# Kernel tuning notes

Measured on AMD Instinct MI355X. Metric: run time of the kernel, lower is better.

Reference implementation:

```python
import jax, jax.numpy as jnp
import numpy as np

N_NODES = 50000


def gcn_conv(x, src, dst, W, b, n_nodes):
    # x: [N, Fin]; src/dst: [E'] (self-loops already included)
    # PyG GCNConv: h = x @ W; aggregate with norm = deg^{-1/2}[src] * deg^{-1/2}[dst]; + bias
    ones = jnp.ones(src.shape[0], dtype=x.dtype)
    deg = jax.ops.segment_sum(ones, dst, num_segments=n_nodes)  # [N]
    dinv = jnp.where(deg > 0, jax.lax.rsqrt(deg), 0.0)
    norm = dinv[src] * dinv[dst]  # [E']
    h = x @ W  # [N, Fout]
    msgs = h[src] * norm[:, None]  # gather + scale, [E', Fout]
    out = jax.ops.segment_sum(msgs, dst, num_segments=n_nodes)  # scatter-add
    return out + b


def setup_inputs() -> dict:
    key = jax.random.key(0)
    ks = jax.random.split(key, 8)
    n, e = N_NODES, 800000
    in_c, out_c = 64, 32
    hid = 2 * out_c  # 64

    def glorot(k, fan_in, fan_out):
        s = jnp.sqrt(2.0 / (fan_in + fan_out))
        return jax.random.normal(k, (fan_in, fan_out), dtype=jnp.float32) * s

    return {
        "z": jax.random.normal(ks[0], (n, in_c), dtype=jnp.float32),
        "edge_index": jax.random.randint(ks[1], (2, e), 0, n, dtype=jnp.int32),
        "W1": glorot(ks[2], in_c, hid),
        "b1": jnp.zeros((hid,), dtype=jnp.float32),
        "W2": glorot(ks[3], hid, out_c),
        "b2": jnp.zeros((out_c,), dtype=jnp.float32),
        "Wfc": glorot(ks[4], out_c, 1024),
        "bfc": jnp.zeros((1024,), dtype=jnp.float32),
    }


def reference(z, edge_index, W1, b1, W2, b2, Wfc, bfc):
    n = z.shape[0]
    # add self-loops once (same augmented graph used by both convs)
    loops = jnp.arange(n, dtype=edge_index.dtype)
    src = jnp.concatenate([edge_index[0], loops])
    dst = jnp.concatenate([edge_index[1], loops])

    h = jax.nn.relu(gcn_conv(z, src, dst, W1, b1, n))
    h = gcn_conv(h, src, dst, W2, b2, n)
    return h @ Wfc + bfc
```

## Files before the change

kernel.cpp:

```cpp
#include <hip/hip_runtime.h>


#define TB 256
#define FC_ROWS 32
#define SCHUNK 4096
#define FLAGB (1 << 30)

typedef __attribute__((ext_vector_type(2))) float f32x2;

__device__ __forceinline__ unsigned short f2bf(float f) {
    unsigned u = __float_as_uint(f);
    u += 0x7fffu + ((u >> 16) & 1u);
    return (unsigned short)(u >> 16);
}

__device__ __forceinline__ void bf4_accum(uint2 p, float4& a) {
    a.x += __uint_as_float(p.x << 16);
    a.y += __uint_as_float(p.x & 0xffff0000u);
    a.z += __uint_as_float(p.y << 16);
    a.w += __uint_as_float(p.y & 0xffff0000u);
}


__global__ void k_zero(int4* __restrict__ p, int n4) {
    int i = blockIdx.x * TB + threadIdx.x;
    if (i < n4) p[i] = make_int4(0, 0, 0, 0);
}


__global__ void k_hist(const int* __restrict__ dst, int* __restrict__ cnt,
                       int* __restrict__ slot, int E) {
    int e = blockIdx.x * TB + threadIdx.x;
    if (e < E) slot[e] = atomicAdd(&cnt[dst[e]], 1);
}

__global__ __launch_bounds__(1024)
void k_scanLB(const int* __restrict__ cnt, int* __restrict__ off,
              float* __restrict__ dinv, int* __restrict__ work, int n, int E) {
    __shared__ int wsum[16];
    __shared__ int pfx_s;
    int b = blockIdx.x;
    int i4 = b * SCHUNK + threadIdx.x * 4;
    int lane = threadIdx.x & 63, wid = threadIdx.x >> 6;
    int v0 = 0, v1 = 0, v2 = 0, v3 = 0;
    if (i4 + 3 < n) {
        int4 t = *(const int4*)(cnt + i4);
        v0 = t.x; v1 = t.y; v2 = t.z; v3 = t.w;
    } else {
        if (i4 < n) v0 = cnt[i4];
        if (i4 + 1 < n) v1 = cnt[i4 + 1];
        if (i4 + 2 < n) v2 = cnt[i4 + 2];
        if (i4 + 3 < n) v3 = cnt[i4 + 3];
    }
    if (i4 < n)     dinv[i4]     = rsqrtf((float)(v0 + 1));
    if (i4 + 1 < n) dinv[i4 + 1] = rsqrtf((float)(v1 + 1));
    if (i4 + 2 < n) dinv[i4 + 2] = rsqrtf((float)(v2 + 1));
    if (i4 + 3 < n) dinv[i4 + 3] = rsqrtf((float)(v3 + 1));

    int s = v0 + v1 + v2 + v3;
    int x = s;
#pragma unroll
    for (int ofs = 1; ofs < 64; ofs <<= 1) {
        int t = __shfl_up(x, ofs, 64);
        if (lane >= ofs) x += t;
    }
    if (lane == 63) wsum[wid] = x;
    __syncthreads();
    int wp = 0;
#pragma unroll
    for (int wv = 0; wv < 16; ++wv) wp += (wv < wid) ? wsum[wv] : 0;
    int excl = wp + x - s;

    if (threadIdx.x == 0) {
        int tot = 0;
#pragma unroll
        for (int wv = 0; wv < 16; ++wv) tot += wsum[wv];
        atomicOr(&work[b], tot | FLAGB);
        int pfx = 0;
        for (int j = 0; j < b; ++j) {
            int v;
            do { v = atomicOr(&work[j], 0); } while (!(v & FLAGB));
            pfx += v & (FLAGB - 1);
        }
        pfx_s = pfx;
        if (b == 0) off[n] = E;
    }
    __syncthreads();
    excl += pfx_s;
    if (i4 < n)     off[i4]     = excl;
    if (i4 + 1 < n) off[i4 + 1] = excl + v0;
    if (i4 + 2 < n) off[i4 + 2] = excl + v0 + v1;
    if (i4 + 3 < n) off[i4 + 3] = excl + v0 + v1 + v2;
}

__global__ void k_fill_gemm(const int* __restrict__ src, const int* __restrict__ dst,
                            const int* __restrict__ off, const int* __restrict__ slot,
                            int* __restrict__ eSrc, int E, int fillBlocks,
                            const float* __restrict__ X, const float* __restrict__ W,
                            const float* __restrict__ dinv,
                            unsigned short* __restrict__ Y, int n) {
    __shared__ float Ws[64 * 64];
    __shared__ float Xs[16 * 64];
    if ((int)blockIdx.x < fillBlocks) {
        int e = blockIdx.x * TB + threadIdx.x;
        if (e < E) eSrc[off[dst[e]] + slot[e]] = src[e];
        return;
    }
    int gb = blockIdx.x - fillBlocks;
    for (int i = threadIdx.x; i < 64 * 64; i += TB) Ws[i] = W[i];
    int r0 = gb * 16;
    int rows = min(16, n - r0);
    {
        const float4* Xg = (const float4*)(X + (size_t)r0 * 64);
        float4* Xs4 = (float4*)Xs;
        int tot4 = rows * 16;
        for (int i = threadIdx.x; i < tot4; i += TB) Xs4[i] = Xg[i];
    }
    __syncthreads();
    int c = threadIdx.x & 63;
    int g = threadIdx.x >> 6;
#pragma unroll
    for (int rr = 0; rr < 4; ++rr) {
        int rb = g + rr * 4;
        int r = r0 + rb;
        if (r >= n) break;
        const float* x = Xs + rb * 64;
        float acc = 0.f;
#pragma unroll
        for (int k = 0; k < 64; ++k) acc = fmaf(x[k], Ws[k * 64 + c], acc);
        Y[(size_t)r * 64 + c] = f2bf(acc * dinv[r]);
    }
}


__global__ void k_gemm_64_32(const float* __restrict__ X, const float* __restrict__ W,
                             const float* __restrict__ dinv,
                             unsigned short* __restrict__ Y, int n) {
    __shared__ float Ws[64 * 32];
    __shared__ float Xs[32 * 64];
    for (int i = threadIdx.x; i < 64 * 32; i += TB) Ws[i] = W[i];
    int r0 = blockIdx.x * 32;
    int rows = min(32, n - r0);
    {
        const float4* Xg = (const float4*)(X + (size_t)r0 * 64);
        float4* Xs4 = (float4*)Xs;
        int tot4 = rows * 16;
        for (int i = threadIdx.x; i < tot4; i += TB) Xs4[i] = Xg[i];
    }
    __syncthreads();
    int c = threadIdx.x & 31;
    int g = threadIdx.x >> 5;
#pragma unroll
    for (int rr = 0; rr < 4; ++rr) {
        int rb = g + rr * 8;
        int r = r0 + rb;
        if (r >= n) break;
        const float* x = Xs + rb * 64;
        float acc = 0.f;
#pragma unroll
        for (int k = 0; k < 64; ++k) acc = fmaf(x[k], Ws[k * 32 + c], acc);
        Y[(size_t)r * 32 + c] = f2bf(acc * dinv[r]);
    }
}


__global__ void k_agg64(const uint2* __restrict__ H2, const int* __restrict__ off,
                        const int* __restrict__ eSrc, const float* __restrict__ dinv,
                        const float4* __restrict__ b4, float4* __restrict__ out4, int n) {
    int node = blockIdx.x * 16 + (threadIdx.x >> 4);
    if (node >= n) return;
    int feat4 = threadIdx.x & 15;
    int j0 = off[node], j1 = off[node + 1];
    float4 a0 = make_float4(0.f, 0.f, 0.f, 0.f);
    float4 a1 = make_float4(0.f, 0.f, 0.f, 0.f);
    float4 a2 = make_float4(0.f, 0.f, 0.f, 0.f);
    float4 a3 = make_float4(0.f, 0.f, 0.f, 0.f);
    int e = j0;
    for (; e + 4 <= j1; e += 4) {
        int s0 = eSrc[e], s1 = eSrc[e + 1], s2 = eSrc[e + 2], s3 = eSrc[e + 3];
        uint2 v0 = H2[(size_t)s0 * 16 + feat4];
        uint2 v1 = H2[(size_t)s1 * 16 + feat4];
        uint2 v2 = H2[(size_t)s2 * 16 + feat4];
        uint2 v3 = H2[(size_t)s3 * 16 + feat4];
        bf4_accum(v0, a0);
        bf4_accum(v1, a1);
        bf4_accum(v2, a2);
        bf4_accum(v3, a3);
    }
    for (; e < j1; ++e) bf4_accum(H2[(size_t)eSrc[e] * 16 + feat4], a0);
    float4 self = make_float4(0.f, 0.f, 0.f, 0.f);
    bf4_accum(H2[(size_t)node * 16 + feat4], self);
    float dv = dinv[node];
    float4 bb = b4[feat4];
    float4 r;
    r.x = fmaxf(fmaf((a0.x + a1.x) + (a2.x + a3.x) + self.x, dv, bb.x), 0.f);
    r.y = fmaxf(fmaf((a0.y + a1.y) + (a2.y + a3.y) + self.y, dv, bb.y), 0.f);
    r.z = fmaxf(fmaf((a0.z + a1.z) + (a2.z + a3.z) + self.z, dv, bb.z), 0.f);
    r.w = fmaxf(fmaf((a0.w + a1.w) + (a2.w + a3.w) + self.w, dv, bb.w), 0.f);
    out4[(size_t)node * 16 + feat4] = r;
}

__global__ void k_agg32(const uint2* __restrict__ H2, const int* __restrict__ off,
                        const int* __restrict__ eSrc, const float* __restrict__ dinv,
                        const float4* __restrict__ b4, float4* __restrict__ out4, int n) {
    int node = blockIdx.x * 32 + (threadIdx.x >> 3);
    if (node >= n) return;
    int feat4 = threadIdx.x & 7;
    int j0 = off[node], j1 = off[node + 1];
    float4 a0 = make_float4(0.f, 0.f, 0.f, 0.f);
    float4 a1 = make_float4(0.f, 0.f, 0.f, 0.f);
    float4 a2 = make_float4(0.f, 0.f, 0.f, 0.f);
    float4 a3 = make_float4(0.f, 0.f, 0.f, 0.f);
    int e = j0;
    for (; e + 4 <= j1; e += 4) {
        int s0 = eSrc[e], s1 = eSrc[e + 1], s2 = eSrc[e + 2], s3 = eSrc[e + 3];
        uint2 v0 = H2[(size_t)s0 * 8 + feat4];
        uint2 v1 = H2[(size_t)s1 * 8 + feat4];
        uint2 v2 = H2[(size_t)s2 * 8 + feat4];
        uint2 v3 = H2[(size_t)s3 * 8 + feat4];
        bf4_accum(v0, a0);
        bf4_accum(v1, a1);
        bf4_accum(v2, a2);
        bf4_accum(v3, a3);
    }
    for (; e < j1; ++e) bf4_accum(H2[(size_t)eSrc[e] * 8 + feat4], a0);
    float4 self = make_float4(0.f, 0.f, 0.f, 0.f);
    bf4_accum(H2[(size_t)node * 8 + feat4], self);
    float dv = dinv[node];
    float4 bb = b4[feat4];
    float4 r;
    r.x = fmaf((a0.x + a1.x) + (a2.x + a3.x) + self.x, dv, bb.x);
    r.y = fmaf((a0.y + a1.y) + (a2.y + a3.y) + self.y, dv, bb.y);
    r.z = fmaf((a0.z + a1.z) + (a2.z + a3.z) + self.z, dv, bb.z);
    r.w = fmaf((a0.w + a1.w) + (a2.w + a3.w) + self.w, dv, bb.w);
    out4[(size_t)node * 8 + feat4] = r;
}

__global__ __launch_bounds__(TB, 4)
void k_fc2(const float* __restrict__ X, const float* __restrict__ W,
           const float* __restrict__ bias, float* __restrict__ Y, int n) {
    __shared__ float Xs[FC_ROWS * 32];
    int c0 = blockIdx.x * 512 + threadIdx.x * 2;
    int r0 = blockIdx.y * FC_ROWS;
    int rows = min(FC_ROWS, n - r0);

    f32x2 w[32];
#pragma unroll
    for (int k = 0; k < 32; ++k) w[k] = *(const f32x2*)(W + k * 1024 + c0);
    f32x2 bb = *(const f32x2*)(bias + c0);

    {
        const float4* Xg = (const float4*)(X + (size_t)r0 * 32);
        float4* Xs4 = (float4*)Xs;
        int tot4 = rows * 8;
        for (int i = threadIdx.x; i < tot4; i += TB) Xs4[i] = Xg[i];
    }
    __syncthreads();

    for (int r = 0; r < rows; ++r) {
        const float* x = Xs + r * 32;
        float a0 = bb.x, a1 = bb.y;
#pragma unroll
        for (int k = 0; k < 32; ++k) {
            float xv = x[k];
            a0 = fmaf(xv, w[k].x, a0);
            a1 = fmaf(xv, w[k].y, a1);
        }
        f32x2 v;
        v.x = a0; v.y = a1;
        __builtin_nontemporal_store(v, (f32x2*)(Y + (size_t)(r0 + r) * 1024 + c0));
    }
}


extern "C" void kernel_launch(void* const* d_in, const int* in_sizes, int n_in,
                              void* d_out, int out_size, void* d_ws, size_t ws_size,
                              hipStream_t stream) {
    const float* z   = (const float*)d_in[0];
    const int*   ei  = (const int*)d_in[1];
    const float* W1  = (const float*)d_in[2];
    const float* b1  = (const float*)d_in[3];
    const float* W2  = (const float*)d_in[4];
    const float* b2  = (const float*)d_in[5];
    const float* Wfc = (const float*)d_in[6];
    const float* bfc = (const float*)d_in[7];
    float* out = (float*)d_out;

    int n = in_sizes[0] / 64;
    int E = in_sizes[1] / 2;
    const int* src = ei;
    const int* dst = ei + E;

    int nPad = (n + 3) & ~3;
    int* cnt    = (int*)d_ws;
    int* work   = cnt + nPad;
    int* off    = work + 16;
    int* slot   = off + ((n + 1 + 3) & ~3);
    int* eSrc   = slot + E;
    float* dinv = (float*)(eSrc + E);
    unsigned short* h1b = (unsigned short*)(dinv + n);
    float* bufB = (float*)(dinv + n + (size_t)n * 32);
    unsigned short* h2b = (unsigned short*)(bufB + (size_t)n * 64);
    float* agg2 = bufB + (size_t)n * 64 + (size_t)n * 16;

    int nChunks = (n + SCHUNK - 1) / SCHUNK;

    {
        int n4 = (nPad + 16) / 4;
        k_zero<<<(n4 + TB - 1) / TB, TB, 0, stream>>>((int4*)cnt, n4);
    }
    k_hist<<<(E + TB - 1) / TB, TB, 0, stream>>>(dst, cnt, slot, E);
    k_scanLB<<<nChunks, 1024, 0, stream>>>(cnt, off, dinv, work, n, E);

    {
        int fillBlocks = (E + TB - 1) / TB;
        int gemmBlocks = (n + 15) / 16;
        k_fill_gemm<<<fillBlocks + gemmBlocks, TB, 0, stream>>>(
            src, dst, off, slot, eSrc, E, fillBlocks, z, W1, dinv, h1b, n);
    }

    k_agg64<<<(n + 15) / 16, TB, 0, stream>>>((const uint2*)h1b, off, eSrc, dinv,
                                              (const float4*)b1, (float4*)bufB, n);

    k_gemm_64_32<<<(n + 31) / 32, TB, 0, stream>>>(bufB, W2, dinv, h2b, n);
    k_agg32<<<(n + 31) / 32, TB, 0, stream>>>((const uint2*)h2b, off, eSrc, dinv,
                                              (const float4*)b2, (float4*)agg2, n);

    {
        dim3 grid(2, (n + FC_ROWS - 1) / FC_ROWS);
        k_fc2<<<grid, TB, 0, stream>>>(agg2, Wfc, bfc, out, n);
    }
}
```

Baseline: 186.7 us.

## Fuse layer-1 aggregation with W2 GEMM and layer-2 aggregation with FC

The first aggregation now computes its ReLU'd rows into shared memory and immediately applies the 64x32 W2 projection, writing bf16 h2 directly. The second aggregation writes its 32-wide rows into shared memory and the same 512-thread block then computes the 1024-column output projection. This removes two intermediate fp32 buffers and two kernel launches. In exchange, each block serializes its gather phase before its dense phase, and the FC block shape changes to 512 threads covering all columns for 64 rows.

```diff
diff --git a/kernel.cpp b/kernel.cpp
--- a/kernel.cpp
+++ b/kernel.cpp
@@ -2,7 +2,7 @@
 
 
 #define TB 256
-#define FC_ROWS 32
+#define FCTB 512
 #define SCHUNK 4096
 #define FLAGB (1 << 30)
 
@@ -132,131 +132,103 @@
     }
 }
 
-
-__global__ void k_gemm_64_32(const float* __restrict__ X, const float* __restrict__ W,
-                             const float* __restrict__ dinv,
-                             unsigned short* __restrict__ Y, int n) {
-    __shared__ float Ws[64 * 32];
-    __shared__ float Xs[32 * 64];
-    for (int i = threadIdx.x; i < 64 * 32; i += TB) Ws[i] = W[i];
-    int r0 = blockIdx.x * 32;
-    int rows = min(32, n - r0);
-    {
-        const float4* Xg = (const float4*)(X + (size_t)r0 * 64);
-        float4* Xs4 = (float4*)Xs;
-        int tot4 = rows * 16;
-        for (int i = threadIdx.x; i < tot4; i += TB) Xs4[i] = Xg[i];
-    }
-    __syncthreads();
-    int c = threadIdx.x & 31;
-    int g = threadIdx.x >> 5;
-#pragma unroll
-    for (int rr = 0; rr < 4; ++rr) {
-        int rb = g + rr * 8;
-        int r = r0 + rb;
-        if (r >= n) break;
-        const float* x = Xs + rb * 64;
-        float acc = 0.f;
-#pragma unroll
-        for (int k = 0; k < 64; ++k) acc = fmaf(x[k], Ws[k * 32 + c], acc);
-        Y[(size_t)r * 32 + c] = f2bf(acc * dinv[r]);
-    }
-}
-
-
-__global__ void k_agg64(const uint2* __restrict__ H2, const int* __restrict__ off,
-                        const int* __restrict__ eSrc, const float* __restrict__ dinv,
-                        const float4* __restrict__ b4, float4* __restrict__ out4, int n) {
-    int node = blockIdx.x * 16 + (threadIdx.x >> 4);
-    if (node >= n) return;
+__global__ void k_agg64g2(const uint2* __restrict__ H2, const int* __restrict__ off,
+                          const int* __restrict__ eSrc, const float* __restrict__ dinv,
+                          const float4* __restrict__ b4, const float* __restrict__ W2,
+                          unsigned short* __restrict__ h2b, int n) {
+    __shared__ float rowsS[16 * 64];
+    __shared__ float W2s[64 * 32];
+    for (int i = threadIdx.x; i < 64 * 32; i += TB) W2s[i] = W2[i];
+    int r0 = blockIdx.x * 16;
+    int node = r0 + (threadIdx.x >> 4);
     int feat4 = threadIdx.x & 15;
-    int j0 = off[node], j1 = off[node + 1];
-    float4 a0 = make_float4(0.f, 0.f, 0.f, 0.f);
-    float4 a1 = make_float4(0.f, 0.f, 0.f, 0.f);
-    float4 a2 = make_float4(0.f, 0.f, 0.f, 0.f);
-    float4 a3 = make_float4(0.f, 0.f, 0.f, 0.f);
-    int e = j0;
-    for (; e + 4 <= j1; e += 4) {
-        int s0 = eSrc[e], s1 = eSrc[e + 1], s2 = eSrc[e + 2], s3 = eSrc[e + 3];
-        uint2 v0 = H2[(size_t)s0 * 16 + feat4];
-        uint2 v1 = H2[(size_t)s1 * 16 + feat4];
-        uint2 v2 = H2[(size_t)s2 * 16 + feat4];
-        uint2 v3 = H2[(size_t)s3 * 16 + feat4];
-        bf4_accum(v0, a0);
-        bf4_accum(v1, a1);
-        bf4_accum(v2, a2);
-        bf4_accum(v3, a3);
-    }
-    for (; e < j1; ++e) bf4_accum(H2[(size_t)eSrc[e] * 16 + feat4], a0);
-    float4 self = make_float4(0.f, 0.f, 0.f, 0.f);
-    bf4_accum(H2[(size_t)node * 16 + feat4], self);
-    float dv = dinv[node];
-    float4 bb = b4[feat4];
-    float4 r;
-    r.x = fmaxf(fmaf((a0.x + a1.x) + (a2.x + a3.x) + self.x, dv, bb.x), 0.f);
-    r.y = fmaxf(fmaf((a0.y + a1.y) + (a2.y + a3.y) + self.y, dv, bb.y), 0.f);
-    r.z = fmaxf(fmaf((a0.z + a1.z) + (a2.z + a3.z) + self.z, dv, bb.z), 0.f);
-    r.w = fmaxf(fmaf((a0.w + a1.w) + (a2.w + a3.w) + self.w, dv, bb.w), 0.f);
-    out4[(size_t)node * 16 + feat4] = r;
-}
-
-__global__ void k_agg32(const uint2* __restrict__ H2, const int* __restrict__ off,
-                        const int* __restrict__ eSrc, const float* __restrict__ dinv,
-                        const float4* __restrict__ b4, float4* __restrict__ out4, int n) {
-    int node = blockIdx.x * 32 + (threadIdx.x >> 3);
-    if (node >= n) return;
+    if (node < n) {
+        int j0 = off[node], j1 = off[node + 1];
+        float4 a0 = make_float4(0.f, 0.f, 0.f, 0.f);
+        float4 a1 = make_float4(0.f, 0.f, 0.f, 0.f);
+        float4 a2 = make_float4(0.f, 0.f, 0.f, 0.f);
+        float4 a3 = make_float4(0.f, 0.f, 0.f, 0.f);
+        int e = j0;
+        for (; e + 4 <= j1; e += 4) {
+            int s0 = eSrc[e], s1 = eSrc[e + 1], s2 = eSrc[e + 2], s3 = eSrc[e + 3];
+            bf4_accum(H2[(size_t)s0 * 16 + feat4], a0);
+            bf4_accum(H2[(size_t)s1 * 16 + feat4], a1);
+            bf4_accum(H2[(size_t)s2 * 16 + feat4], a2);
+            bf4_accum(H2[(size_t)s3 * 16 + feat4], a3);
+        }
+        for (; e < j1; ++e) bf4_accum(H2[(size_t)eSrc[e] * 16 + feat4], a0);
+        float4 self = make_float4(0.f, 0.f, 0.f, 0.f);
+        bf4_accum(H2[(size_t)node * 16 + feat4], self);
+        float dv = dinv[node];
+        float4 bb = b4[feat4];
+        float4 r;
+        r.x = fmaxf(fmaf((a0.x + a1.x) + (a2.x + a3.x) + self.x, dv, bb.x), 0.f);
+        r.y = fmaxf(fmaf((a0.y + a1.y) + (a2.y + a3.y) + self.y, dv, bb.y), 0.f);
+        r.z = fmaxf(fmaf((a0.z + a1.z) + (a2.z + a3.z) + self.z, dv, bb.z), 0.f);
+        r.w = fmaxf(fmaf((a0.w + a1.w) + (a2.w + a3.w) + self.w, dv, bb.w), 0.f);
+        ((float4*)rowsS)[(threadIdx.x >> 4) * 16 + feat4] = r;
+    }
+    __syncthreads();
+#pragma unroll
+    for (int rep = 0; rep < 2; ++rep) {
+        int idx = rep * TB + threadIdx.x;
+        int nd = idx >> 5, c = idx & 31;
+        int gn = r0 + nd;
+        if (gn < n) {
+            const float* x = rowsS + nd * 64;
+            float acc = 0.f;
+#pragma unroll
+            for (int k = 0; k < 64; ++k) acc = fmaf(x[k], W2s[k * 32 + c], acc);
+            h2b[(size_t)gn * 32 + c] = f2bf(acc * dinv[gn]);
+        }
+    }
+}
+
+__global__ __launch_bounds__(FCTB, 4)
+void k_aggfc(const uint2* __restrict__ H2, const int* __restrict__ off,
+             const int* __restrict__ eSrc, const float* __restrict__ dinv,
+             const float4* __restrict__ b4, const float* __restrict__ Wfc,
+             const float* __restrict__ bfc, float* __restrict__ Y, int n) {
+    __shared__ float Xs[64 * 32];
+    int r0 = blockIdx.x * 64;
+    int c0 = threadIdx.x * 2;
+
+    f32x2 w[32];
+#pragma unroll
+    for (int k = 0; k < 32; ++k) w[k] = *(const f32x2*)(Wfc + k * 1024 + c0);
+    f32x2 bb = *(const f32x2*)(bfc + c0);
+
+    int node = r0 + (threadIdx.x >> 3);
     int feat4 = threadIdx.x & 7;
-    int j0 = off[node], j1 = off[node + 1];
-    float4 a0 = make_float4(0.f, 0.f, 0.f, 0.f);
-    float4 a1 = make_float4(0.f, 0.f, 0.f, 0.f);
-    float4 a2 = make_float4(0.f, 0.f, 0.f, 0.f);
-    float4 a3 = make_float4(0.f, 0.f, 0.f, 0.f);
-    int e = j0;
-    for (; e + 4 <= j1; e += 4) {
-        int s0 = eSrc[e], s1 = eSrc[e + 1], s2 = eSrc[e + 2], s3 = eSrc[e + 3];
-        uint2 v0 = H2[(size_t)s0 * 8 + feat4];
-        uint2 v1 = H2[(size_t)s1 * 8 + feat4];
-        uint2 v2 = H2[(size_t)s2 * 8 + feat4];
-        uint2 v3 = H2[(size_t)s3 * 8 + feat4];
-        bf4_accum(v0, a0);
-        bf4_accum(v1, a1);
-        bf4_accum(v2, a2);
-        bf4_accum(v3, a3);
-    }
-    for (; e < j1; ++e) bf4_accum(H2[(size_t)eSrc[e] * 8 + feat4], a0);
-    float4 self = make_float4(0.f, 0.f, 0.f, 0.f);
-    bf4_accum(H2[(size_t)node * 8 + feat4], self);
-    float dv = dinv[node];
-    float4 bb = b4[feat4];
-    float4 r;
-    r.x = fmaf((a0.x + a1.x) + (a2.x + a3.x) + self.x, dv, bb.x);
-    r.y = fmaf((a0.y + a1.y) + (a2.y + a3.y) + self.y, dv, bb.y);
-    r.z = fmaf((a0.z + a1.z) + (a2.z + a3.z) + self.z, dv, bb.z);
-    r.w = fmaf((a0.w + a1.w) + (a2.w + a3.w) + self.w, dv, bb.w);
-    out4[(size_t)node * 8 + feat4] = r;
-}
-
-__global__ __launch_bounds__(TB, 4)
-void k_fc2(const float* __restrict__ X, const float* __restrict__ W,
-           const float* __restrict__ bias, float* __restrict__ Y, int n) {
-    __shared__ float Xs[FC_ROWS * 32];
-    int c0 = blockIdx.x * 512 + threadIdx.x * 2;
-    int r0 = blockIdx.y * FC_ROWS;
-    int rows = min(FC_ROWS, n - r0);
-
-    f32x2 w[32];
-#pragma unroll
-    for (int k = 0; k < 32; ++k) w[k] = *(const f32x2*)(W + k * 1024 + c0);
-    f32x2 bb = *(const f32x2*)(bias + c0);
-
-    {
-        const float4* Xg = (const float4*)(X + (size_t)r0 * 32);
-        float4* Xs4 = (float4*)Xs;
-        int tot4 = rows * 8;
-        for (int i = threadIdx.x; i < tot4; i += TB) Xs4[i] = Xg[i];
-    }
-    __syncthreads();
-
+    if (node < n) {
+        int j0 = off[node], j1 = off[node + 1];
+        float4 a0 = make_float4(0.f, 0.f, 0.f, 0.f);
+        float4 a1 = make_float4(0.f, 0.f, 0.f, 0.f);
+        float4 a2 = make_float4(0.f, 0.f, 0.f, 0.f);
+        float4 a3 = make_float4(0.f, 0.f, 0.f, 0.f);
+        int e = j0;
+        for (; e + 4 <= j1; e += 4) {
+            int s0 = eSrc[e], s1 = eSrc[e + 1], s2 = eSrc[e + 2], s3 = eSrc[e + 3];
+            bf4_accum(H2[(size_t)s0 * 8 + feat4], a0);
+            bf4_accum(H2[(size_t)s1 * 8 + feat4], a1);
+            bf4_accum(H2[(size_t)s2 * 8 + feat4], a2);
+            bf4_accum(H2[(size_t)s3 * 8 + feat4], a3);
+        }
+        for (; e < j1; ++e) bf4_accum(H2[(size_t)eSrc[e] * 8 + feat4], a0);
+        float4 self = make_float4(0.f, 0.f, 0.f, 0.f);
+        bf4_accum(H2[(size_t)node * 8 + feat4], self);
+        float dv = dinv[node];
+        float4 cb = b4[feat4];
+        float4 r;
+        r.x = fmaf((a0.x + a1.x) + (a2.x + a3.x) + self.x, dv, cb.x);
+        r.y = fmaf((a0.y + a1.y) + (a2.y + a3.y) + self.y, dv, cb.y);
+        r.z = fmaf((a0.z + a1.z) + (a2.z + a3.z) + self.z, dv, cb.z);
+        r.w = fmaf((a0.w + a1.w) + (a2.w + a3.w) + self.w, dv, cb.w);
+        ((float4*)Xs)[(threadIdx.x >> 3) * 8 + feat4] = r;
+    }
+    __syncthreads();
+
+    int rows = min(64, n - r0);
     for (int r = 0; r < rows; ++r) {
         const float* x = Xs + r * 32;
         float a0 = bb.x, a1 = bb.y;
@@ -292,16 +264,15 @@
     const int* dst = ei + E;
 
     int nPad = (n + 3) & ~3;
+    int ePad = (E + 3) & ~3;
     int* cnt    = (int*)d_ws;
     int* work   = cnt + nPad;
     int* off    = work + 16;
     int* slot   = off + ((n + 1 + 3) & ~3);
-    int* eSrc   = slot + E;
-    float* dinv = (float*)(eSrc + E);
-    unsigned short* h1b = (unsigned short*)(dinv + n);
-    float* bufB = (float*)(dinv + n + (size_t)n * 32);
-    unsigned short* h2b = (unsigned short*)(bufB + (size_t)n * 64);
-    float* agg2 = bufB + (size_t)n * 64 + (size_t)n * 16;
+    int* eSrc   = slot + ePad;
+    float* dinv = (float*)(eSrc + ePad);
+    unsigned short* h1b = (unsigned short*)(dinv + nPad);
+    unsigned short* h2b = (unsigned short*)(dinv + nPad + (size_t)n * 32);
 
     int nChunks = (n + SCHUNK - 1) / SCHUNK;
 
@@ -319,15 +290,9 @@
             src, dst, off, slot, eSrc, E, fillBlocks, z, W1, dinv, h1b, n);
     }
 
-    k_agg64<<<(n + 15) / 16, TB, 0, stream>>>((const uint2*)h1b, off, eSrc, dinv,
-                                              (const float4*)b1, (float4*)bufB, n);
-
-    k_gemm_64_32<<<(n + 31) / 32, TB, 0, stream>>>(bufB, W2, dinv, h2b, n);
-    k_agg32<<<(n + 31) / 32, TB, 0, stream>>>((const uint2*)h2b, off, eSrc, dinv,
-                                              (const float4*)b2, (float4*)agg2, n);
-
-    {
-        dim3 grid(2, (n + FC_ROWS - 1) / FC_ROWS);
-        k_fc2<<<grid, TB, 0, stream>>>(agg2, Wfc, bfc, out, n);
-    }
-}
+    k_agg64g2<<<(n + 15) / 16, TB, 0, stream>>>((const uint2*)h1b, off, eSrc, dinv,
+                                                (const float4*)b1, W2, h2b, n);
+
+    k_aggfc<<<(n + 63) / 64, FCTB, 0, stream>>>((const uint2*)h2b, off, eSrc, dinv,
+                                                (const float4*)b2, Wfc, bfc, out, n);
+}
```

Result: no change. 183.5 us (-1.7%).
